# Kernel tuning notes

Hardware: AMD Instinct MI355X
Metric: run time of the kernel (lower is better)

Reference implementation:

```python
import jax, jax.numpy as jnp
import numpy as np

N_NODES = 100000
N_EDGES = 1600000
D = 64

def setup_inputs() -> dict:
    key = jax.random.key(0)
    k1, k2, k3, k4 = jax.random.split(key, 4)
    feat = jax.random.normal(k1, (N_NODES, D), dtype=jnp.float32)
    src = jax.random.randint(k2, (N_EDGES,), 0, N_NODES, dtype=jnp.int32)
    dst = jax.random.randint(k3, (N_EDGES,), 0, N_NODES, dtype=jnp.int32)
    eps = jnp.zeros((1,), dtype=jnp.float32)
    W = jax.random.normal(k4, (D, D), dtype=jnp.float32) * (1.0 / np.sqrt(D))
    b = jnp.zeros((D,), dtype=jnp.float32)
    return {"feat": feat, "src": src, "dst": dst, "eps": eps, "W": W, "b": b}

def reference(feat, src, dst, eps, W, b):
    # GIN: h_i = f_Theta((1+eps)*h_i + sum_{j in N(i)} h_j)
    # Neighbor gather + segment-sum aggregation over edges (sum aggregator).
    msgs = feat[src]  # [E, D] gather of source node features
    agg = jax.ops.segment_sum(msgs, dst, num_segments=N_NODES)  # [N, D]
    rst = (1.0 + eps[0]) * feat + agg  # (1+eps)*self + aggregate
    # apply_func: Linear(D, D)
    return rst @ W + b
```

## Files before the change

### kernel.cpp

```cpp
#include <hip/hip_runtime.h>

#define NN 100000
#define NE 1600000
#define DD 64

#define NPB 128
#define NBUCK ((NN + NPB - 1) / NPB)
#define CAP 3072
#define OVF_CAP 4096
#define CHUNK 2048
#define NPART ((NE + CHUNK - 1) / CHUNK)


__global__ void __launch_bounds__(256) partition3_kernel(
    const int* __restrict__ src, const int* __restrict__ dst,
    int* __restrict__ gcur, int* __restrict__ ovf_cnt, int* __restrict__ ovf,
    unsigned int* __restrict__ sorted) {
  __shared__ int hist[NBUCK];
  __shared__ int base[NBUCK];
  int tid = threadIdx.x;
  int chunk = blockIdx.x * CHUNK;

  for (int i = tid; i < NBUCK; i += 256) hist[i] = 0;
  __syncthreads();

#pragma unroll
  for (int i = 0; i < CHUNK / 256; ++i) {
    int e = chunk + i * 256 + tid;
    if (e < NE) atomicAdd(&hist[dst[e] >> 7], 1);
  }
  __syncthreads();

  for (int i = tid; i < NBUCK; i += 256) {
    int h = hist[i];
    base[i] = h ? atomicAdd(&gcur[i], h) : 0;
  }
  __syncthreads();

#pragma unroll
  for (int i = 0; i < CHUNK / 256; ++i) {
    int e = chunk + i * 256 + tid;
    if (e < NE) {
      int s = src[e], d = dst[e];
      int bk = d >> 7;
      int r = atomicAdd(&base[bk], 1);
      if (r < CAP) {
        sorted[bk * CAP + r] = ((unsigned int)s << 7) | (unsigned int)(d & 127);
      } else {
        int oi = atomicAdd(ovf_cnt, 1);
        if (oi < OVF_CAP) { ovf[2 * oi] = s; ovf[2 * oi + 1] = d; }
      }
    }
  }
}

__global__ void __launch_bounds__(256) bucket_agg2_kernel(
    const float* __restrict__ feat, const float* __restrict__ eps,
    const int* __restrict__ gcur, const unsigned int* __restrict__ sorted,
    float* __restrict__ out) {
  __shared__ int lhist[NPB];
  __shared__ int loffs[NPB];
  __shared__ int lcur[NPB];
  __shared__ int srcs[CAP];
  int tid = threadIdx.x;
  int bk = blockIdx.x;
  int base = bk * CAP;
  int cnt = gcur[bk];
  if (cnt > CAP) cnt = CAP;
  const float4* f4 = reinterpret_cast<const float4*>(feat);

  if (tid < NPB) lhist[tid] = 0;
  __syncthreads();

  for (int i = tid; i < cnt; i += 256)
    atomicAdd(&lhist[sorted[base + i] & 127], 1);
  __syncthreads();

  if (tid < NPB) loffs[tid] = lhist[tid];
  __syncthreads();
  for (int off = 1; off < NPB; off <<= 1) {
    int t = 0;
    if (tid < NPB && tid >= off) t = loffs[tid - off];
    __syncthreads();
    if (tid < NPB) loffs[tid] += t;
    __syncthreads();
  }
  if (tid < NPB) lcur[tid] = loffs[tid] - lhist[tid];
  __syncthreads();

  for (int i = tid; i < cnt; i += 256) {
    unsigned int rec = sorted[base + i];
    int pos = atomicAdd(&lcur[rec & 127], 1);
    srcs[pos] = (int)(rec >> 7);
  }
  __syncthreads();

  float ec = 1.0f + eps[0];
  int grp = tid >> 4, q = tid & 15;
  int node0 = bk * NPB;
  for (int ln = grp; ln < NPB; ln += 16) {
    int row = node0 + ln;
    if (row >= NN) break;
    int s = loffs[ln] - lhist[ln];
    int e2 = loffs[ln];
    float4 sf = f4[(size_t)row * 16 + q];
    float ax = ec * sf.x, ay = ec * sf.y, az = ec * sf.z, aw = ec * sf.w;
    int k = s;
    for (; k + 4 <= e2; k += 4) {
      int s0 = srcs[k + 0], s1 = srcs[k + 1], s2 = srcs[k + 2], s3 = srcs[k + 3];
      float4 v0 = f4[(size_t)s0 * 16 + q];
      float4 v1 = f4[(size_t)s1 * 16 + q];
      float4 v2 = f4[(size_t)s2 * 16 + q];
      float4 v3 = f4[(size_t)s3 * 16 + q];
      ax += (v0.x + v1.x) + (v2.x + v3.x);
      ay += (v0.y + v1.y) + (v2.y + v3.y);
      az += (v0.z + v1.z) + (v2.z + v3.z);
      aw += (v0.w + v1.w) + (v2.w + v3.w);
    }
    for (; k < e2; ++k) {
      int s4i = srcs[k];
      float4 v = f4[(size_t)s4i * 16 + q];
      ax += v.x; ay += v.y; az += v.z; aw += v.w;
    }
    reinterpret_cast<float4*>(out)[(size_t)row * 16 + q] =
        make_float4(ax, ay, az, aw);
  }
}

__global__ void __launch_bounds__(256) row_gemm4_kernel(
    float* __restrict__ out, const float* __restrict__ W,
    const float* __restrict__ b, const int* __restrict__ ovf_cnt,
    const int* __restrict__ ovf, const float* __restrict__ feat) {
  int lane = threadIdx.x & 63;
  int wid  = threadIdx.x >> 6;
  int g = blockIdx.x * 4 + wid;
  int row0 = g * 8;

  float w[64];
#pragma unroll
  for (int k = 0; k < 64; ++k) w[k] = W[k * DD + lane];
  float bv = b[lane];

  float rstv[8], acc[8];
#pragma unroll
  for (int r = 0; r < 8; ++r) rstv[r] = out[(size_t)(row0 + r) * DD + lane];

  int novf = ovf_cnt[0];
  if (novf > 0) {
    if (novf > OVF_CAP) novf = OVF_CAP;
    for (int i = 0; i < novf; ++i) {
      int d = ovf[2 * i + 1];
      int r = d - row0;
      if (r >= 0 && r < 8) rstv[r] += feat[(size_t)ovf[2 * i] * DD + lane];
    }
  }

#pragma unroll
  for (int r = 0; r < 8; ++r) acc[r] = bv;
#pragma unroll
  for (int k = 0; k < 64; ++k) {
#pragma unroll
    for (int r = 0; r < 8; ++r) {
      float s = __uint_as_float(__builtin_amdgcn_readlane(__float_as_uint(rstv[r]), k));
      acc[r] = fmaf(s, w[k], acc[r]);
    }
  }
#pragma unroll
  for (int r = 0; r < 8; ++r) out[(size_t)(row0 + r) * DD + lane] = acc[r];
}

__global__ void __launch_bounds__(256) row_gemm3_kernel(float* __restrict__ out,
                                                        const float* __restrict__ W,
                                                        const float* __restrict__ b) {
  int lane = threadIdx.x & 63;
  int wid  = threadIdx.x >> 6;
  int g = blockIdx.x * 4 + wid;
  if (g >= NN / 16) return;
  int row0 = g * 16;

  float w[64];
#pragma unroll
  for (int k = 0; k < 64; ++k) w[k] = W[k * DD + lane];
  float bv = b[lane];

#pragma unroll
  for (int batch = 0; batch < 2; ++batch) {
    int rbase = row0 + batch * 8;
    float rstv[8], acc[8];
#pragma unroll
    for (int r = 0; r < 8; ++r) rstv[r] = out[(size_t)(rbase + r) * DD + lane];
#pragma unroll
    for (int r = 0; r < 8; ++r) acc[r] = bv;
#pragma unroll
    for (int k = 0; k < 64; ++k) {
#pragma unroll
      for (int r = 0; r < 8; ++r) {
        float s = __uint_as_float(__builtin_amdgcn_readlane(__float_as_uint(rstv[r]), k));
        acc[r] = fmaf(s, w[k], acc[r]);
      }
    }
#pragma unroll
    for (int r = 0; r < 8; ++r) out[(size_t)(rbase + r) * DD + lane] = acc[r];
  }
}


constexpr int NB_SCAN = (NN + 1023) / 1024;

__global__ void __launch_bounds__(256) zero_kernel(int* __restrict__ p, int n) {
  int i = blockIdx.x * blockDim.x + threadIdx.x;
  if (i < n) p[i] = 0;
}

__global__ void __launch_bounds__(256) hist_kernel(const int* __restrict__ dst,
                                                   int* __restrict__ count) {
  int e = blockIdx.x * blockDim.x + threadIdx.x;
  atomicAdd(&count[dst[e]], 1);
}

__global__ void __launch_bounds__(1024) scan1_kernel(const int* __restrict__ count,
                                                     int* __restrict__ offsets,
                                                     int* __restrict__ bsums) {
  __shared__ int tmp[1024];
  int tid = threadIdx.x;
  int gid = blockIdx.x * 1024 + tid;
  int v = (gid < NN) ? count[gid] : 0;
  tmp[tid] = v;
  __syncthreads();
  for (int off = 1; off < 1024; off <<= 1) {
    int t = (tid >= off) ? tmp[tid - off] : 0;
    __syncthreads();
    tmp[tid] += t;
    __syncthreads();
  }
  if (gid < NN) offsets[gid] = tmp[tid] - v;
  if (tid == 1023) bsums[blockIdx.x] = tmp[1023];
}

__global__ void __launch_bounds__(128) scan2_kernel(int* __restrict__ bsums) {
  __shared__ int tmp[128];
  int tid = threadIdx.x;
  int v = (tid < NB_SCAN) ? bsums[tid] : 0;
  tmp[tid] = v;
  __syncthreads();
  for (int off = 1; off < 128; off <<= 1) {
    int t = (tid >= off) ? tmp[tid - off] : 0;
    __syncthreads();
    tmp[tid] += t;
    __syncthreads();
  }
  if (tid < NB_SCAN) bsums[tid] = tmp[tid] - v;
}

__global__ void __launch_bounds__(256) scan3_kernel(int* __restrict__ offsets,
                                                    const int* __restrict__ bsums,
                                                    int* __restrict__ cursor) {
  int gid = blockIdx.x * blockDim.x + threadIdx.x;
  if (gid < NN) {
    int o = offsets[gid] + bsums[gid >> 10];
    offsets[gid] = o;
    cursor[gid] = o;
  } else if (gid == NN) {
    offsets[NN] = NE;
  }
}

__global__ void __launch_bounds__(256) place_kernel(const int* __restrict__ src,
                                                    const int* __restrict__ dst,
                                                    int* __restrict__ cursor,
                                                    int* __restrict__ sorted) {
  int e = blockIdx.x * blockDim.x + threadIdx.x;
  int p = atomicAdd(&cursor[dst[e]], 1);
  sorted[p] = src[e];
}

__global__ void __launch_bounds__(256) pull4_kernel(const float* __restrict__ feat,
                                                    const float* __restrict__ eps,
                                                    const int* __restrict__ offsets,
                                                    const int* __restrict__ sorted,
                                                    float* __restrict__ out) {
  int t = blockIdx.x * blockDim.x + threadIdx.x;
  int node = t >> 4;
  int q = t & 15;
  const float4* f4 = reinterpret_cast<const float4*>(feat);

  int start = offsets[node];
  int end   = offsets[node + 1];
  float e = 1.0f + eps[0];
  float4 self = f4[(size_t)node * 16 + q];
  float ax = e * self.x, ay = e * self.y, az = e * self.z, aw = e * self.w;

  int k = start;
  for (; k + 4 <= end; k += 4) {
    int s0 = sorted[k + 0], s1 = sorted[k + 1], s2 = sorted[k + 2], s3 = sorted[k + 3];
    float4 v0 = f4[(size_t)s0 * 16 + q];
    float4 v1 = f4[(size_t)s1 * 16 + q];
    float4 v2 = f4[(size_t)s2 * 16 + q];
    float4 v3 = f4[(size_t)s3 * 16 + q];
    ax += (v0.x + v1.x) + (v2.x + v3.x);
    ay += (v0.y + v1.y) + (v2.y + v3.y);
    az += (v0.z + v1.z) + (v2.z + v3.z);
    aw += (v0.w + v1.w) + (v2.w + v3.w);
  }
  for (; k < end; ++k) {
    int s = sorted[k];
    float4 v = f4[(size_t)s * 16 + q];
    ax += v.x; ay += v.y; az += v.z; aw += v.w;
  }

  reinterpret_cast<float4*>(out)[(size_t)node * 16 + q] = make_float4(ax, ay, az, aw);
}


__global__ void __launch_bounds__(256) init_out_kernel(const float* __restrict__ feat,
                                                       const float* __restrict__ eps,
                                                       float* __restrict__ out) {
  int i = blockIdx.x * blockDim.x + threadIdx.x;
  float e = 1.0f + eps[0];
  float4 f = reinterpret_cast<const float4*>(feat)[i];
  reinterpret_cast<float4*>(out)[i] = make_float4(e * f.x, e * f.y, e * f.z, e * f.w);
}

__global__ void __launch_bounds__(256) scatter_edges_kernel(const float* __restrict__ feat,
                                                            const int* __restrict__ src,
                                                            const int* __restrict__ dst,
                                                            float* __restrict__ out) {
  int t = blockIdx.x * blockDim.x + threadIdx.x;
  int e = t >> 4;
  int q = t & 15;
  int s = src[e];
  int d = dst[e];
  float4 v = reinterpret_cast<const float4*>(feat)[s * 16 + q];
  float* op = out + d * DD + q * 4;
  atomicAdd(op + 0, v.x);
  atomicAdd(op + 1, v.y);
  atomicAdd(op + 2, v.z);
  atomicAdd(op + 3, v.w);
}


extern "C" void kernel_launch(void* const* d_in, const int* in_sizes, int n_in,
                              void* d_out, int out_size, void* d_ws, size_t ws_size,
                              hipStream_t stream) {
  const float* feat = (const float*)d_in[0];
  const int* src    = (const int*)d_in[1];
  const int* dst    = (const int*)d_in[2];
  const float* eps  = (const float*)d_in[3];
  const float* W    = (const float*)d_in[4];
  const float* b    = (const float*)d_in[5];
  float* out        = (float*)d_out;

  const size_t needA = ((size_t)NBUCK + 2 + 2 * OVF_CAP + (size_t)NBUCK * CAP) * sizeof(int);
  const size_t needB = ((size_t)3 * NN + 136 + NE) * sizeof(int);

  if (ws_size >= needA) {
    int* wsI = (int*)d_ws;
    int* gcur    = wsI;
    int* ovf_cnt = wsI + NBUCK;
    int* ovf     = wsI + NBUCK + 2;
    unsigned int* sorted = (unsigned int*)(wsI + NBUCK + 2 + 2 * OVF_CAP);

    hipMemsetAsync(gcur, 0, (NBUCK + 2) * sizeof(int), stream);
    partition3_kernel<<<NPART, 256, 0, stream>>>(src, dst, gcur, ovf_cnt, ovf, sorted);
    bucket_agg2_kernel<<<NBUCK, 256, 0, stream>>>(feat, eps, gcur, sorted, out);
    row_gemm4_kernel<<<NN / 8 / 4, 256, 0, stream>>>(out, W, b, ovf_cnt, ovf, feat);
  } else if (ws_size >= needB) {
    int* wsI     = (int*)d_ws;
    int* count   = wsI;
    int* offsets = wsI + NN;
    int* cursor  = wsI + 2 * NN + 8;
    int* bsums   = wsI + 3 * NN + 8;
    int* sortedB = wsI + 3 * NN + 136;

    zero_kernel<<<(NN + 255) / 256, 256, 0, stream>>>(count, NN);
    hist_kernel<<<NE / 256, 256, 0, stream>>>(dst, count);
    scan1_kernel<<<NB_SCAN, 1024, 0, stream>>>(count, offsets, bsums);
    scan2_kernel<<<1, 128, 0, stream>>>(bsums);
    scan3_kernel<<<(NN + 1 + 255) / 256, 256, 0, stream>>>(offsets, bsums, cursor);
    place_kernel<<<NE / 256, 256, 0, stream>>>(src, dst, cursor, sortedB);
    pull4_kernel<<<(NN * 16) / 256, 256, 0, stream>>>(feat, eps, offsets, sortedB, out);
    row_gemm3_kernel<<<(NN / 16 + 3) / 4, 256, 0, stream>>>(out, W, b);
  } else {
    init_out_kernel<<<(NN * DD / 4) / 256, 256, 0, stream>>>(feat, eps, out);
    scatter_edges_kernel<<<(NE * 16) / 256, 256, 0, stream>>>(feat, src, dst, out);
    row_gemm3_kernel<<<(NN / 16 + 3) / 4, 256, 0, stream>>>(out, W, b);
  }
}
```

Baseline: 217.0 us.

## Enlarge partition chunks, split bucket aggregation launch, widen GEMM rows per wave

Doubles the partition chunk and block size to 512 threads, so fewer blocks do global atomics on the bucket cursors. Splits bucket aggregation into two launches over halves of the buckets, using a bucket offset parameter and a bounds check. Replaces the row GEMM with a variant that handles 16 rows per wave in two batches of 8, so the per-lane W registers are loaded once for twice as many rows. These are several unrelated tweaks, and the extra launch adds overhead while larger chunks reduce parallelism in partitioning.

```diff
diff --git a/kernel.cpp b/kernel.cpp
--- a/kernel.cpp
+++ b/kernel.cpp
@@ -8,11 +8,12 @@
 #define NBUCK ((NN + NPB - 1) / NPB)
 #define CAP 3072
 #define OVF_CAP 4096
-#define CHUNK 2048
+#define CHUNK 4096
 #define NPART ((NE + CHUNK - 1) / CHUNK)
-
-
-__global__ void __launch_bounds__(256) partition3_kernel(
+#define PTHREADS 512
+
+
+__global__ void __launch_bounds__(PTHREADS) partition3_kernel(
     const int* __restrict__ src, const int* __restrict__ dst,
     int* __restrict__ gcur, int* __restrict__ ovf_cnt, int* __restrict__ ovf,
     unsigned int* __restrict__ sorted) {
@@ -21,25 +22,25 @@
   int tid = threadIdx.x;
   int chunk = blockIdx.x * CHUNK;
 
-  for (int i = tid; i < NBUCK; i += 256) hist[i] = 0;
-  __syncthreads();
-
-#pragma unroll
-  for (int i = 0; i < CHUNK / 256; ++i) {
-    int e = chunk + i * 256 + tid;
+  for (int i = tid; i < NBUCK; i += PTHREADS) hist[i] = 0;
+  __syncthreads();
+
+#pragma unroll
+  for (int i = 0; i < CHUNK / PTHREADS; ++i) {
+    int e = chunk + i * PTHREADS + tid;
     if (e < NE) atomicAdd(&hist[dst[e] >> 7], 1);
   }
   __syncthreads();
 
-  for (int i = tid; i < NBUCK; i += 256) {
+  for (int i = tid; i < NBUCK; i += PTHREADS) {
     int h = hist[i];
     base[i] = h ? atomicAdd(&gcur[i], h) : 0;
   }
   __syncthreads();
 
 #pragma unroll
-  for (int i = 0; i < CHUNK / 256; ++i) {
-    int e = chunk + i * 256 + tid;
+  for (int i = 0; i < CHUNK / PTHREADS; ++i) {
+    int e = chunk + i * PTHREADS + tid;
     if (e < NE) {
       int s = src[e], d = dst[e];
       int bk = d >> 7;
@@ -57,13 +58,14 @@
 __global__ void __launch_bounds__(256) bucket_agg2_kernel(
     const float* __restrict__ feat, const float* __restrict__ eps,
     const int* __restrict__ gcur, const unsigned int* __restrict__ sorted,
-    float* __restrict__ out) {
+    float* __restrict__ out, int bk0) {
   __shared__ int lhist[NPB];
   __shared__ int loffs[NPB];
   __shared__ int lcur[NPB];
   __shared__ int srcs[CAP];
   int tid = threadIdx.x;
-  int bk = blockIdx.x;
+  int bk = bk0 + blockIdx.x;
+  if (bk >= NBUCK) return;
   int base = bk * CAP;
   int cnt = gcur[bk];
   if (cnt > CAP) cnt = CAP;
@@ -127,46 +129,52 @@
   }
 }
 
-__global__ void __launch_bounds__(256) row_gemm4_kernel(
+__global__ void __launch_bounds__(256) row_gemm5_kernel(
     float* __restrict__ out, const float* __restrict__ W,
     const float* __restrict__ b, const int* __restrict__ ovf_cnt,
     const int* __restrict__ ovf, const float* __restrict__ feat) {
   int lane = threadIdx.x & 63;
   int wid  = threadIdx.x >> 6;
   int g = blockIdx.x * 4 + wid;
-  int row0 = g * 8;
+  if (g >= NN / 16) return;
+  int row0 = g * 16;
 
   float w[64];
 #pragma unroll
   for (int k = 0; k < 64; ++k) w[k] = W[k * DD + lane];
   float bv = b[lane];
 
-  float rstv[8], acc[8];
-#pragma unroll
-  for (int r = 0; r < 8; ++r) rstv[r] = out[(size_t)(row0 + r) * DD + lane];
-
   int novf = ovf_cnt[0];
-  if (novf > 0) {
-    if (novf > OVF_CAP) novf = OVF_CAP;
-    for (int i = 0; i < novf; ++i) {
-      int d = ovf[2 * i + 1];
-      int r = d - row0;
-      if (r >= 0 && r < 8) rstv[r] += feat[(size_t)ovf[2 * i] * DD + lane];
-    }
-  }
-
-#pragma unroll
-  for (int r = 0; r < 8; ++r) acc[r] = bv;
-#pragma unroll
-  for (int k = 0; k < 64; ++k) {
-#pragma unroll
-    for (int r = 0; r < 8; ++r) {
-      float s = __uint_as_float(__builtin_amdgcn_readlane(__float_as_uint(rstv[r]), k));
-      acc[r] = fmaf(s, w[k], acc[r]);
-    }
-  }
-#pragma unroll
-  for (int r = 0; r < 8; ++r) out[(size_t)(row0 + r) * DD + lane] = acc[r];
+  if (novf > OVF_CAP) novf = OVF_CAP;
+
+#pragma unroll
+  for (int batch = 0; batch < 2; ++batch) {
+    int rbase = row0 + batch * 8;
+    float rstv[8], acc[8];
+#pragma unroll
+    for (int r = 0; r < 8; ++r) rstv[r] = out[(size_t)(rbase + r) * DD + lane];
+
+    if (novf > 0) {
+      for (int i = 0; i < novf; ++i) {
+        int d = ovf[2 * i + 1];
+        int r = d - rbase;
+        if (r >= 0 && r < 8) rstv[r] += feat[(size_t)ovf[2 * i] * DD + lane];
+      }
+    }
+
+#pragma unroll
+    for (int r = 0; r < 8; ++r) acc[r] = bv;
+#pragma unroll
+    for (int k = 0; k < 64; ++k) {
+#pragma unroll
+      for (int r = 0; r < 8; ++r) {
+        float s = __uint_as_float(__builtin_amdgcn_readlane(__float_as_uint(rstv[r]), k));
+        acc[r] = fmaf(s, w[k], acc[r]);
+      }
+    }
+#pragma unroll
+    for (int r = 0; r < 8; ++r) out[(size_t)(rbase + r) * DD + lane] = acc[r];
+  }
 }
 
 __global__ void __launch_bounds__(256) row_gemm3_kernel(float* __restrict__ out,
@@ -361,9 +369,11 @@
     unsigned int* sorted = (unsigned int*)(wsI + NBUCK + 2 + 2 * OVF_CAP);
 
     hipMemsetAsync(gcur, 0, (NBUCK + 2) * sizeof(int), stream);
-    partition3_kernel<<<NPART, 256, 0, stream>>>(src, dst, gcur, ovf_cnt, ovf, sorted);
-    bucket_agg2_kernel<<<NBUCK, 256, 0, stream>>>(feat, eps, gcur, sorted, out);
-    row_gemm4_kernel<<<NN / 8 / 4, 256, 0, stream>>>(out, W, b, ovf_cnt, ovf, feat);
+    partition3_kernel<<<NPART, PTHREADS, 0, stream>>>(src, dst, gcur, ovf_cnt, ovf, sorted);
+    const int half = (NBUCK + 1) / 2;
+    bucket_agg2_kernel<<<half, 256, 0, stream>>>(feat, eps, gcur, sorted, out, 0);
+    bucket_agg2_kernel<<<NBUCK - half, 256, 0, stream>>>(feat, eps, gcur, sorted, out, half);
+    row_gemm5_kernel<<<(NN / 16 + 3) / 4, 256, 0, stream>>>(out, W, b, ovf_cnt, ovf, feat);
   } else if (ws_size >= needB) {
     int* wsI     = (int*)d_ws;
     int* count   = wsI;
```

Result: no change. 218.2 us (+0.6%).
